# Kernel tuning notes

Hardware: AMD Instinct MI355X
Metric: run time of the kernel (lower is better)

The kernel has to match this reference:

```python
import jax, jax.numpy as jnp
import numpy as np

D_MODEL = 64
D_K = 64
D_V = 64
N_HEADS = 4
D_FF = 64
D_HALF = 32  # d_model / 2 in the sca_* MLPs


def _layer_norm(x, eps=1e-5):
    m = jnp.mean(x, axis=-1, keepdims=True)
    v = jnp.var(x, axis=-1, keepdims=True)
    return (x - m) / jnp.sqrt(v + eps)


def _sca(u, w1, w2):
    # nn.Sequential(Linear(64,32), ReLU, Linear(32,1)), no bias
    return jax.nn.relu(u @ w1) @ w2  # [B,1,1]


def setup_inputs() -> dict:
    key = jax.random.key(0)
    ks = jax.random.split(key, 20)
    B, L = 128, 512

    def lin(k, fan_in, fan_out):
        bound = 1.0 / np.sqrt(fan_in)
        return jax.random.uniform(k, (fan_in, fan_out), jnp.float32, -bound, bound)

    inp = {
        "input": jax.random.normal(ks[0], (B, L, D_MODEL), jnp.float32),
        "attn_mask": jax.random.bernoulli(ks[1], 0.1, (B, L, L)),
        "input_u": jax.random.normal(ks[2], (B, 1, D_MODEL), jnp.float32),
        "W_Q": lin(ks[3], D_MODEL, N_HEADS * D_K),
        "W_K": lin(ks[4], D_MODEL, N_HEADS * D_K),
        "W_V": lin(ks[5], D_MODEL, N_HEADS * D_V),
        "U_Q": lin(ks[6], D_MODEL, D_K),
        "U_K": lin(ks[7], D_MODEL, D_K),
        "U_V": lin(ks[8], D_MODEL, D_V),
        "sq1": lin(ks[9], D_MODEL, D_HALF),
        "sq2": lin(ks[10], D_HALF, 1),
        "sk1": lin(ks[11], D_MODEL, D_HALF),
        "sk2": lin(ks[12], D_HALF, 1),
        "sv1": lin(ks[13], D_MODEL, D_HALF),
        "sv2": lin(ks[14], D_HALF, 1),
        "fc": lin(ks[15], N_HEADS * D_V, D_MODEL),
        "ff1": lin(ks[16], D_MODEL, D_FF),
        "ff2": lin(ks[17], D_FF, D_MODEL),
    }
    return inp


def reference(input, attn_mask, input_u, W_Q, W_K, W_V, U_Q, U_K, U_V,
              sq1, sq2, sk1, sk2, sv1, sv2, fc, ff1, ff2):
    B, L, _ = input.shape
    scale = 1.0 / np.sqrt(D_K).astype(np.float32)

    # multi-head projections: [B, H, L, d]
    Q = (input @ W_Q).reshape(B, L, N_HEADS, D_K).transpose(0, 2, 1, 3)
    K = (input @ W_K).reshape(B, L, N_HEADS, D_K).transpose(0, 2, 1, 3)
    V = (input @ W_V).reshape(B, L, N_HEADS, D_V).transpose(0, 2, 1, 3)

    # per-batch scalar gates from input_u: [B,1,1]
    s_q = _sca(input_u, sq1, sq2)
    s_k = _sca(input_u, sk1, sk2)
    s_v = _sca(input_u, sv1, sv2)

    # single-head u projections, gated; broadcast over heads later
    u_Q = (input @ U_Q) * s_q  # [B, L, d_k]
    u_K = (input @ U_K) * s_k  # [B, L, d_k]
    u_V = (input @ U_V) * s_v  # [B, L, d_v]

    scores = jnp.einsum('bhqd,bhkd->bhqk', Q, K) * scale
    scores = scores + (jnp.einsum('bqd,bkd->bqk', u_Q, u_K) * scale)[:, None]
    scores = jnp.where(attn_mask[:, None], jnp.float32(-1e9), scores)
    attn = jax.nn.softmax(scores, axis=-1)  # [B, H, L, L]

    context = jnp.einsum('bhqk,bhkd->bhqd', attn, V + u_V[:, None])
    context = context.transpose(0, 2, 1, 3).reshape(B, L, N_HEADS * D_V)

    out = context @ fc  # dropout is identity in eval
    enc = _layer_norm(out + input)

    # position-wise FFN with residual + layernorm
    ffn = jax.nn.relu(enc @ ff1) @ ff2
    enc_outputs = _layer_norm(ffn + enc)
    return (enc_outputs, attn)
```

## Files before the change

kernel.cpp:

```cpp
#include <hip/hip_runtime.h>

typedef unsigned char  u8;
typedef unsigned short u16;
typedef unsigned int   u32;

typedef __attribute__((ext_vector_type(8))) short bf16x8;
typedef __attribute__((ext_vector_type(4))) float f32x4;

__device__ __forceinline__ u16 f2bf(float f) {
  union { float f; u32 u; } v; v.f = f;
  u32 u = v.u;
  u32 r = u + 0x7fffu + ((u >> 16) & 1u);
  return (u16)(r >> 16);
}
__device__ __forceinline__ bf16x8 pack8(float4 a, float4 b) {
  bf16x8 r;
  r[0] = (short)f2bf(a.x); r[1] = (short)f2bf(a.y);
  r[2] = (short)f2bf(a.z); r[3] = (short)f2bf(a.w);
  r[4] = (short)f2bf(b.x); r[5] = (short)f2bf(b.y);
  r[6] = (short)f2bf(b.z); r[7] = (short)f2bf(b.w);
  return r;
}
__device__ __forceinline__ f32x4 mfma16(bf16x8 a, bf16x8 b, f32x4 c) {
  return __builtin_amdgcn_mfma_f32_16x16x32_bf16(a, b, c, 0, 0, 0);
}

__global__ void kflaginit(u32* flags) { flags[0] = 0; flags[1] = 0; }

__global__ void kscan(const u32* __restrict__ m, u32* __restrict__ flags) {
  int gid = blockIdx.x * 256 + threadIdx.x;
  const uint4* p = (const uint4*)m;
  u32 gt = 0, fp = 0;
#pragma unroll
  for (int i = 0; i < 4; ++i) {
    uint4 v = p[gid * 4 + i];
    gt |= (u32)((v.x > 1u) | (v.y > 1u) | (v.z > 1u) | (v.w > 1u));
    fp |= (u32)((v.x == 0x3F800000u) | (v.y == 0x3F800000u) |
                (v.z == 0x3F800000u) | (v.w == 0x3F800000u));
  }
  if (gt) flags[0] = 1;
  if (fp) flags[1] = 1;
}

__global__ void kconv(const void* __restrict__ m, const u32* __restrict__ flags,
                      u8* __restrict__ out) {
  int gid = blockIdx.x * 256 + threadIdx.x;
  u32 isf = flags[1], isb = flags[0];
  uchar4 o;
  if (isf) {
    float4 v = ((const float4*)m)[gid];
    o.x = v.x != 0.f; o.y = v.y != 0.f; o.z = v.z != 0.f; o.w = v.w != 0.f;
  } else if (isb) {
    uchar4 v = ((const uchar4*)m)[gid];
    o.x = v.x != 0; o.y = v.y != 0; o.z = v.z != 0; o.w = v.w != 0;
  } else {
    uint4 v = ((const uint4*)m)[gid];
    o.x = v.x != 0; o.y = v.y != 0; o.z = v.z != 0; o.w = v.w != 0;
  }
  ((uchar4*)out)[gid] = o;
}

__global__ void kprep(const float* __restrict__ wq, const float* __restrict__ wk,
                      const float* __restrict__ wv, const float* __restrict__ uq,
                      const float* __restrict__ uk, const float* __restrict__ uv,
                      const float* __restrict__ fc, const float* __restrict__ f1,
                      const float* __restrict__ f2, const float* __restrict__ iu,
                      const float* __restrict__ q1, const float* __restrict__ q2,
                      const float* __restrict__ k1, const float* __restrict__ k2,
                      const float* __restrict__ v1, const float* __restrict__ v2,
                      u16* __restrict__ wqT, u16* __restrict__ wkT, u16* __restrict__ wvT,
                      u16* __restrict__ uqT, u16* __restrict__ ukT, u16* __restrict__ uvT,
                      u16* __restrict__ fcT, u16* __restrict__ f1T, u16* __restrict__ f2T,
                      float* __restrict__ gates) {
  int bid = blockIdx.x, t = threadIdx.x;
  if (bid < 3) {
    const float* src = bid == 0 ? wq : bid == 1 ? wk : wv;
    u16* dst = bid == 0 ? wqT : bid == 1 ? wkT : wvT;
    for (int i = 0; i < 64; ++i) {
      int e = t + i * 256; int n = e & 255, k = e >> 8;
      dst[n * 64 + k] = f2bf(src[k * 256 + n]);
    }
  } else if (bid < 6) {
    const float* src = bid == 3 ? uq : bid == 4 ? uk : uv;
    u16* dst = bid == 3 ? uqT : bid == 4 ? ukT : uvT;
    for (int i = 0; i < 16; ++i) {
      int e = t + i * 256; int n = e & 63, k = e >> 6;
      dst[n * 64 + k] = f2bf(src[k * 64 + n]);
    }
  } else if (bid == 6) {
    for (int i = 0; i < 64; ++i) {
      int e = t + i * 256; int n = e & 63, k = e >> 6;
      fcT[n * 256 + k] = f2bf(fc[k * 64 + n]);
    }
  } else if (bid == 7) {
    for (int i = 0; i < 16; ++i) {
      int e = t + i * 256; int n = e & 63, k = e >> 6;
      f1T[n * 64 + k] = f2bf(f1[k * 64 + n]);
    }
  } else if (bid == 8) {
    for (int i = 0; i < 16; ++i) {
      int e = t + i * 256; int n = e & 63, k = e >> 6;
      f2T[n * 64 + k] = f2bf(f2[k * 64 + n]);
    }
  } else {
    int b = bid - 9;
    __shared__ float u[64];
    if (t < 64) u[t] = iu[b * 64 + t];
    __syncthreads();
    if (t < 64) {
      const float* w1[3] = {q1, k1, v1};
      const float* w2[3] = {q2, k2, v2};
#pragma unroll
      for (int m = 0; m < 3; ++m) {
        float p = 0.f;
        if (t < 32) {
          float h = 0.f;
          for (int i = 0; i < 64; ++i) h += u[i] * w1[m][i * 32 + t];
          p = fmaxf(h, 0.f) * w2[m][t];
        }
        for (int off = 32; off >= 1; off >>= 1) p += __shfl_xor(p, off);
        if (t == 0) gates[m * 128 + b] = p;
      }
    }
  }
}

__launch_bounds__(256, 2)
__global__ void kproj_qk(const float* __restrict__ x,
                         const u16* __restrict__ wqT, const u16* __restrict__ uqT,
                         const u16* __restrict__ wkT, const u16* __restrict__ ukT,
                         const float* __restrict__ gates,
                         u16* __restrict__ qc, u16* __restrict__ qu,
                         u16* __restrict__ kc, u16* __restrict__ ku) {
  __shared__ u16 XT[64 * 136];
  int b = blockIdx.x >> 3, l0 = (blockIdx.x & 7) * 64, t = threadIdx.x;
  {
    int tok = t >> 2, i0 = (t & 3) * 16;
    const float4* s = (const float4*)(x + ((size_t)(b * 512 + l0 + tok)) * 64 + i0);
    *(bf16x8*)&XT[tok * 136 + i0]     = pack8(s[0], s[1]);
    *(bf16x8*)&XT[tok * 136 + i0 + 8] = pack8(s[2], s[3]);
  }
  __syncthreads();

  int w = t >> 6, lane = t & 63, lrow = lane & 15, lgrp = lane >> 4;
  bf16x8 af[4][2];
#pragma unroll
  for (int m = 0; m < 4; ++m)
#pragma unroll
    for (int fs = 0; fs < 2; ++fs)
      af[m][fs] = *(const bf16x8*)&XT[(m * 16 + lrow) * 136 + fs * 32 + lgrp * 8];

  float sq = gates[b], sk = gates[128 + b];
  const f32x4 fz = {0.f, 0.f, 0.f, 0.f};
#pragma unroll
  for (int part = 0; part < 2; ++part) {
    const u16* WT = part ? wkT : wqT;
    const u16* UT = part ? ukT : uqT;
    f32x4 acc[4][5];
#pragma unroll
    for (int m = 0; m < 4; ++m)
#pragma unroll
      for (int nt = 0; nt < 5; ++nt) acc[m][nt] = fz;
#pragma unroll
    for (int fs = 0; fs < 2; ++fs)
#pragma unroll
      for (int nt = 0; nt < 5; ++nt) {
        const u16* src = (nt < 4) ? WT + (w * 64 + nt * 16 + lrow) * 64
                                  : UT + (w * 16 + lrow) * 64;
        bf16x8 bf = *(const bf16x8*)(src + fs * 32 + lgrp * 8);
#pragma unroll
        for (int m = 0; m < 4; ++m)
          acc[m][nt] = mfma16(af[m][fs], bf, acc[m][nt]);
      }
    u16* dstC = part ? kc : qc;
    u16* dstU = part ? ku : qu;
    float presc = part ? 1.0f : 0.125f;
    float gg = (part ? sk : sq) * presc;
#pragma unroll
    for (int nt = 0; nt < 5; ++nt) {
#pragma unroll
      for (int m = 0; m < 4; ++m)
#pragma unroll
        for (int j = 0; j < 4; ++j) {
          int l = l0 + m * 16 + lgrp * 4 + j;
          float v = acc[m][nt][j];
          if (nt < 4) {
            int ncol = w * 64 + nt * 16 + lrow;
            dstC[(((size_t)(b * 4 + (ncol >> 6)) * 512) + l) * 64 + (ncol & 63)] = (short)f2bf(v * presc);
          } else {
            int uc = w * 16 + lrow;
            dstU[((size_t)b * 512 + l) * 64 + uc] = (short)f2bf(v * gg);
          }
        }
    }
  }
}

__launch_bounds__(256, 2)
__global__ void kproj_v(const float* __restrict__ x,
                        const u16* __restrict__ wvT, const u16* __restrict__ uvT,
                        const float* __restrict__ gates, u16* __restrict__ vpt) {
  __shared__ u16 XT[64 * 136];
  __shared__ float Vs[64 * 329];
  int b = blockIdx.x >> 3, l0 = (blockIdx.x & 7) * 64, t = threadIdx.x;
  {
    int tok = t >> 2, i0 = (t & 3) * 16;
    const float4* s = (const float4*)(x + ((size_t)(b * 512 + l0 + tok)) * 64 + i0);
    *(bf16x8*)&XT[tok * 136 + i0]     = pack8(s[0], s[1]);
    *(bf16x8*)&XT[tok * 136 + i0 + 8] = pack8(s[2], s[3]);
  }
  __syncthreads();

  int w = t >> 6, lane = t & 63, lrow = lane & 15, lgrp = lane >> 4;
  bf16x8 af[4][2];
#pragma unroll
  for (int m = 0; m < 4; ++m)
#pragma unroll
    for (int fs = 0; fs < 2; ++fs)
      af[m][fs] = *(const bf16x8*)&XT[(m * 16 + lrow) * 136 + fs * 32 + lgrp * 8];

  const f32x4 fz = {0.f, 0.f, 0.f, 0.f};
  f32x4 acc[4][5];
#pragma unroll
  for (int m = 0; m < 4; ++m)
#pragma unroll
    for (int nt = 0; nt < 5; ++nt) acc[m][nt] = fz;
#pragma unroll
  for (int fs = 0; fs < 2; ++fs)
#pragma unroll
    for (int nt = 0; nt < 5; ++nt) {
      const u16* src = (nt < 4) ? wvT + (w * 64 + nt * 16 + lrow) * 64
                                : uvT + (w * 16 + lrow) * 64;
      bf16x8 bf = *(const bf16x8*)(src + fs * 32 + lgrp * 8);
#pragma unroll
      for (int m = 0; m < 4; ++m)
        acc[m][nt] = mfma16(af[m][fs], bf, acc[m][nt]);
    }
#pragma unroll
  for (int nt = 0; nt < 5; ++nt)
#pragma unroll
    for (int m = 0; m < 4; ++m)
#pragma unroll
      for (int j = 0; j < 4; ++j) {
        int tok = m * 16 + lgrp * 4 + j;
        int col = (nt < 4) ? (w * 64 + nt * 16 + lrow) : (256 + w * 16 + lrow);
        Vs[tok * 329 + col] = acc[m][nt][j];
      }
  __syncthreads();

  float sv = gates[256 + b];
#pragma unroll
  for (int p = 0; p < 4; ++p) {
    int hd = p * 64 + (t >> 2);
    int d = hd & 63;
    int tok0 = (t & 3) * 16;
    bf16x8 v0, v1;
#pragma unroll
    for (int i = 0; i < 8; ++i) {
      int tok = tok0 + i;
      v0[i] = (short)f2bf(Vs[tok * 329 + hd] + Vs[tok * 329 + 256 + d] * sv);
    }
#pragma unroll
    for (int i = 0; i < 8; ++i) {
      int tok = tok0 + 8 + i;
      v1[i] = (short)f2bf(Vs[tok * 329 + hd] + Vs[tok * 329 + 256 + d] * sv);
    }
    size_t base = (((size_t)(b * 4 + (hd >> 6)) * 64) + d) * 512 + l0 + tok0;
    *(bf16x8*)&vpt[base] = v0;
    *(bf16x8*)&vpt[base + 8] = v1;
  }
}

__launch_bounds__(512)
__global__ void __attribute__((amdgpu_waves_per_eu(2, 4)))
kattn(const u16* __restrict__ qc, const u16* __restrict__ qu,
      const u16* __restrict__ kc, const u16* __restrict__ ku,
      const u16* __restrict__ vpt, const u8* __restrict__ maskb,
      float* __restrict__ aout, u16* __restrict__ ctx) {
  __shared__ char smem[35840];
  u16* KT  = (u16*)smem;
  u16* Pl0 = (u16*)smem;
  u16* Pl1 = (u16*)(smem + 17408);
  float* SMm = (float*)(smem + 34816);
  float* SMl = (float*)(smem + 35328);

  int bid = blockIdx.x;
  int logical = (bid & 7) * 512 + (bid >> 3);
  int b = logical >> 5;
  int r5 = logical & 31;
  int qt = r5 >> 2, hh = r5 & 3;
  int bh = b * 4 + hh;
  int q0 = qt * 64;

  int t = threadIdx.x, w = t >> 6, lane = t & 63, lrow = lane & 15, lgrp = lane >> 4;
  int qsub = w & 3, g = w >> 2, g64 = g * 64;
  int qloc0 = qsub * 16 + lgrp * 4;

  bf16x8 qf[4];
  {
    const u16* qrow = qc + ((size_t)bh * 512 + q0 + qsub * 16 + lrow) * 64;
    const u16* urow = qu + ((size_t)b  * 512 + q0 + qsub * 16 + lrow) * 64;
    qf[0] = *(const bf16x8*)(qrow + lgrp * 8);
    qf[1] = *(const bf16x8*)(qrow + 32 + lgrp * 8);
    qf[2] = *(const bf16x8*)(urow + lgrp * 8);
    qf[3] = *(const bf16x8*)(urow + 32 + lgrp * 8);
  }

  int r = t >> 2;
  uint4 kreg[4];
#define LDK(kt)                                                                   \
  {                                                                               \
    _Pragma("unroll")                                                             \
    for (int i = 0; i < 4; ++i) {                                                 \
      int c = (t & 3) * 4 + i;                                                    \
      const u16* src = (c < 8)                                                    \
        ? kc + ((size_t)bh * 512 + (kt) * 128 + r) * 64 + c * 8                   \
        : ku + ((size_t)b  * 512 + (kt) * 128 + r) * 64 + (c - 8) * 8;            \
      kreg[i] = *(const uint4*)src;                                               \
    }                                                                             \
  }

  LDK(0);
  const f32x4 fz = {0.f, 0.f, 0.f, 0.f};
  f32x4 acc[16];
#pragma unroll
  for (int i = 0; i < 16; ++i) acc[i] = fz;

#pragma unroll
  for (int kt = 0; kt < 4; ++kt) {
    __syncthreads();
#pragma unroll
    for (int i = 0; i < 4; ++i)
      *(uint4*)&KT[r * 136 + ((t & 3) * 4 + i) * 8] = kreg[i];
    if (kt < 3) LDK(kt + 1);
    __syncthreads();
#pragma unroll
    for (int fs = 0; fs < 4; ++fs)
#pragma unroll
      for (int nt = 0; nt < 4; ++nt) {
        bf16x8 bf = *(const bf16x8*)&KT[(g64 + nt * 16 + lrow) * 136 + fs * 32 + lgrp * 8];
        acc[kt * 4 + nt] = mfma16(qf[fs], bf, acc[kt * 4 + nt]);
      }
  }

  const u8* mrow = maskb + ((size_t)b * 512 + q0 + qloc0) * 512;
  float mj[4] = {-3.0e38f, -3.0e38f, -3.0e38f, -3.0e38f};
#pragma unroll
  for (int i = 0; i < 16; ++i) {
    int kpos = (i >> 2) * 128 + g64 + (i & 3) * 16 + lrow;
#pragma unroll
    for (int j = 0; j < 4; ++j) {
      float s = acc[i][j];
      if (mrow[(size_t)j * 512 + kpos]) s = -1.0e9f;
      acc[i][j] = s;
      mj[j] = fmaxf(mj[j], s);
    }
  }
#pragma unroll
  for (int j = 0; j < 4; ++j) {
    mj[j] = fmaxf(mj[j], __shfl_xor(mj[j], 1));
    mj[j] = fmaxf(mj[j], __shfl_xor(mj[j], 2));
    mj[j] = fmaxf(mj[j], __shfl_xor(mj[j], 4));
    mj[j] = fmaxf(mj[j], __shfl_xor(mj[j], 8));
  }
  if (lrow == 0) {
#pragma unroll
    for (int j = 0; j < 4; ++j) SMm[g64 + qloc0 + j] = mj[j];
  }
  __syncthreads();
  float gm[4];
#pragma unroll
  for (int j = 0; j < 4; ++j) gm[j] = fmaxf(SMm[qloc0 + j], SMm[64 + qloc0 + j]);
  float lj[4] = {0.f, 0.f, 0.f, 0.f};
#pragma unroll
  for (int i = 0; i < 16; ++i)
#pragma unroll
    for (int j = 0; j < 4; ++j) {
      float p = __expf(acc[i][j] - gm[j]);
      acc[i][j] = p;
      lj[j] += p;
    }
#pragma unroll
  for (int j = 0; j < 4; ++j) {
    lj[j] += __shfl_xor(lj[j], 1);
    lj[j] += __shfl_xor(lj[j], 2);
    lj[j] += __shfl_xor(lj[j], 4);
    lj[j] += __shfl_xor(lj[j], 8);
  }
  if (lrow == 0) {
#pragma unroll
    for (int j = 0; j < 4; ++j) SMl[g64 + qloc0 + j] = lj[j];
  }
  __syncthreads();
  float inv[4];
#pragma unroll
  for (int j = 0; j < 4; ++j) inv[j] = 1.0f / (SMl[qloc0 + j] + SMl[64 + qloc0 + j]);

  size_t ab = ((size_t)bh * 512 + q0 + qloc0) * 512;
  f32x4 cacc[2] = {fz, fz};
#pragma unroll
  for (int c = 0; c < 4; ++c) {
    u16* Pl = (c & 1) ? Pl1 : Pl0;
    bf16x8 vf[4][2];
#pragma unroll
    for (int ks = 0; ks < 4; ++ks)
#pragma unroll
      for (int nt2 = 0; nt2 < 2; ++nt2)
        vf[ks][nt2] = *(const bf16x8*)(vpt + ((size_t)bh * 64 + g * 32 + nt2 * 16 + lrow) * 512
                                       + c * 128 + ks * 32 + lgrp * 8);
#pragma unroll
    for (int nt = 0; nt < 4; ++nt)
#pragma unroll
      for (int j = 0; j < 4; ++j)
        Pl[(qloc0 + j) * 136 + g64 + nt * 16 + lrow] = (short)f2bf(acc[c * 4 + nt][j] * inv[j]);
    __syncthreads();
#pragma unroll
    for (int nt = 0; nt < 4; ++nt)
#pragma unroll
      for (int j = 0; j < 4; ++j)
        aout[ab + (size_t)j * 512 + c * 128 + g64 + nt * 16 + lrow] = acc[c * 4 + nt][j] * inv[j];
#pragma unroll
    for (int ks = 0; ks < 4; ++ks) {
      bf16x8 a = *(const bf16x8*)&Pl[(qsub * 16 + lrow) * 136 + ks * 32 + lgrp * 8];
      cacc[0] = mfma16(a, vf[ks][0], cacc[0]);
      cacc[1] = mfma16(a, vf[ks][1], cacc[1]);
    }
  }
#pragma unroll
  for (int nt2 = 0; nt2 < 2; ++nt2)
#pragma unroll
    for (int j = 0; j < 4; ++j)
      ctx[((size_t)b * 512 + q0 + qloc0 + j) * 256 + hh * 64 + g * 32 + nt2 * 16 + lrow] =
          (short)f2bf(cacc[nt2][j]);
}

__launch_bounds__(256, 2)
__global__ void kffn(const u16* __restrict__ ctx, const float* __restrict__ x,
                     const u16* __restrict__ fcT, const u16* __restrict__ f1T,
                     const u16* __restrict__ f2T, float* __restrict__ out) {
  __shared__ float ENC[64 * 68];
  __shared__ u16 EBF[64 * 72];
  __shared__ u16 HBF[64 * 72];
  int b = blockIdx.x >> 3, l0 = (blockIdx.x & 7) * 64, t = threadIdx.x;
  int w = t >> 6, lane = t & 63, lrow = lane & 15, lgrp = lane >> 4;
  int row = w * 16 + lgrp * 4;
  const f32x4 fz = {0.f, 0.f, 0.f, 0.f};

  f32x4 acc[4];
#pragma unroll
  for (int nt = 0; nt < 4; ++nt) acc[nt] = fz;
#pragma unroll
  for (int ks = 0; ks < 8; ++ks) {
    bf16x8 a = *(const bf16x8*)(ctx + ((size_t)(b * 512 + l0 + w * 16 + lrow)) * 256 + ks * 32 + lgrp * 8);
#pragma unroll
    for (int nt = 0; nt < 4; ++nt) {
      bf16x8 bf = *(const bf16x8*)(fcT + (nt * 16 + lrow) * 256 + ks * 32 + lgrp * 8);
      acc[nt] = mfma16(a, bf, acc[nt]);
    }
  }
  const float* xb = x + ((size_t)(b * 512 + l0)) * 64;
#pragma unroll
  for (int nt = 0; nt < 4; ++nt)
#pragma unroll
    for (int j = 0; j < 4; ++j)
      acc[nt][j] += xb[(row + j) * 64 + nt * 16 + lrow];

  float mean[4], rstd[4];
#pragma unroll
  for (int j = 0; j < 4; ++j) {
    float s = acc[0][j] + acc[1][j] + acc[2][j] + acc[3][j];
    s += __shfl_xor(s, 1); s += __shfl_xor(s, 2); s += __shfl_xor(s, 4); s += __shfl_xor(s, 8);
    mean[j] = s * 0.015625f;
  }
#pragma unroll
  for (int j = 0; j < 4; ++j) {
    float d0 = acc[0][j] - mean[j], d1 = acc[1][j] - mean[j];
    float d2 = acc[2][j] - mean[j], d3 = acc[3][j] - mean[j];
    float s = d0 * d0 + d1 * d1 + d2 * d2 + d3 * d3;
    s += __shfl_xor(s, 1); s += __shfl_xor(s, 2); s += __shfl_xor(s, 4); s += __shfl_xor(s, 8);
    rstd[j] = 1.0f / sqrtf(s * 0.015625f + 1e-5f);
  }
#pragma unroll
  for (int nt = 0; nt < 4; ++nt)
#pragma unroll
    for (int j = 0; j < 4; ++j) {
      float v = (acc[nt][j] - mean[j]) * rstd[j];
      ENC[(row + j) * 68 + nt * 16 + lrow] = v;
      EBF[(row + j) * 72 + nt * 16 + lrow] = (short)f2bf(v);
    }

  f32x4 h4[4];
#pragma unroll
  for (int nt = 0; nt < 4; ++nt) h4[nt] = fz;
#pragma unroll
  for (int ks = 0; ks < 2; ++ks) {
    bf16x8 a = *(const bf16x8*)&EBF[(w * 16 + lrow) * 72 + ks * 32 + lgrp * 8];
#pragma unroll
    for (int nt = 0; nt < 4; ++nt) {
      bf16x8 bf = *(const bf16x8*)(f1T + (nt * 16 + lrow) * 64 + ks * 32 + lgrp * 8);
      h4[nt] = mfma16(a, bf, h4[nt]);
    }
  }
#pragma unroll
  for (int nt = 0; nt < 4; ++nt)
#pragma unroll
    for (int j = 0; j < 4; ++j)
      HBF[(row + j) * 72 + nt * 16 + lrow] = (short)f2bf(fmaxf(h4[nt][j], 0.f));

  f32x4 o4[4];
#pragma unroll
  for (int nt = 0; nt < 4; ++nt) o4[nt] = fz;
#pragma unroll
  for (int ks = 0; ks < 2; ++ks) {
    bf16x8 a = *(const bf16x8*)&HBF[(w * 16 + lrow) * 72 + ks * 32 + lgrp * 8];
#pragma unroll
    for (int nt = 0; nt < 4; ++nt) {
      bf16x8 bf = *(const bf16x8*)(f2T + (nt * 16 + lrow) * 64 + ks * 32 + lgrp * 8);
      o4[nt] = mfma16(a, bf, o4[nt]);
    }
  }
#pragma unroll
  for (int nt = 0; nt < 4; ++nt)
#pragma unroll
    for (int j = 0; j < 4; ++j)
      o4[nt][j] += ENC[(row + j) * 68 + nt * 16 + lrow];

  float mean2[4], rstd2[4];
#pragma unroll
  for (int j = 0; j < 4; ++j) {
    float s = o4[0][j] + o4[1][j] + o4[2][j] + o4[3][j];
    s += __shfl_xor(s, 1); s += __shfl_xor(s, 2); s += __shfl_xor(s, 4); s += __shfl_xor(s, 8);
    mean2[j] = s * 0.015625f;
  }
#pragma unroll
  for (int j = 0; j < 4; ++j) {
    float d0 = o4[0][j] - mean2[j], d1 = o4[1][j] - mean2[j];
    float d2 = o4[2][j] - mean2[j], d3 = o4[3][j] - mean2[j];
    float s = d0 * d0 + d1 * d1 + d2 * d2 + d3 * d3;
    s += __shfl_xor(s, 1); s += __shfl_xor(s, 2); s += __shfl_xor(s, 4); s += __shfl_xor(s, 8);
    rstd2[j] = 1.0f / sqrtf(s * 0.015625f + 1e-5f);
  }
#pragma unroll
  for (int nt = 0; nt < 4; ++nt)
#pragma unroll
    for (int j = 0; j < 4; ++j)
      out[((size_t)(b * 512 + l0) + row + j) * 64 + nt * 16 + lrow] =
          (o4[nt][j] - mean2[j]) * rstd2[j];
}

extern "C" void kernel_launch(void* const* d_in, const int* in_sizes, int n_in,
                              void* d_out, int out_size, void* d_ws, size_t ws_size,
                              hipStream_t stream) {
  const float* x   = (const float*)d_in[0];
  const void*  msk = d_in[1];
  const float* iu  = (const float*)d_in[2];
  const float* wq  = (const float*)d_in[3];
  const float* wk  = (const float*)d_in[4];
  const float* wv  = (const float*)d_in[5];
  const float* uq  = (const float*)d_in[6];
  const float* uk  = (const float*)d_in[7];
  const float* uv  = (const float*)d_in[8];
  const float* q1  = (const float*)d_in[9];
  const float* q2  = (const float*)d_in[10];
  const float* k1  = (const float*)d_in[11];
  const float* k2  = (const float*)d_in[12];
  const float* v1  = (const float*)d_in[13];
  const float* v2  = (const float*)d_in[14];
  const float* fcw = (const float*)d_in[15];
  const float* f1w = (const float*)d_in[16];
  const float* f2w = (const float*)d_in[17];
  float* out = (float*)d_out;

  char* ws = (char*)d_ws;
  u32*   flags = (u32*)ws;
  float* gates = (float*)(ws + 64);
  u16* wqT = (u16*)(ws + 4096);
  u16* wkT = (u16*)(ws + 36864);
  u16* wvT = (u16*)(ws + 69632);
  u16* uqT = (u16*)(ws + 102400);
  u16* ukT = (u16*)(ws + 110592);
  u16* uvT = (u16*)(ws + 118784);
  u16* fcT = (u16*)(ws + 126976);
  u16* f1T = (u16*)(ws + 159744);
  u16* f2T = (u16*)(ws + 167936);
  u16* qc  = (u16*)(ws + 180224);
  u16* qu  = (u16*)(ws + 33734656);
  u16* kc  = (u16*)(ws + 42123264);
  u16* ku  = (u16*)(ws + 75677696);
  u16* vpt = (u16*)(ws + 84066304);
  u8*  mb  = (u8*) (ws + 117620736);
  u16* ctx = (u16*)(ws + 151175168);

  kflaginit<<<dim3(1), dim3(1), 0, stream>>>(flags);
  kscan<<<dim3(1024), dim3(256), 0, stream>>>((const u32*)msk, flags);
  kconv<<<dim3(32768), dim3(256), 0, stream>>>(msk, flags, mb);
  kprep<<<dim3(137), dim3(256), 0, stream>>>(wq, wk, wv, uq, uk, uv, fcw, f1w, f2w,
                                             iu, q1, q2, k1, k2, v1, v2,
                                             wqT, wkT, wvT, uqT, ukT, uvT, fcT, f1T, f2T, gates);
  kproj_qk<<<dim3(1024), dim3(256), 0, stream>>>(x, wqT, uqT, wkT, ukT, gates, qc, qu, kc, ku);
  kproj_v<<<dim3(1024), dim3(256), 0, stream>>>(x, wvT, uvT, gates, vpt);
  kattn<<<dim3(4096), dim3(512), 0, stream>>>(qc, qu, kc, ku, vpt, mb, out + 4194304, ctx);
  kffn<<<dim3(1024), dim3(256), 0, stream>>>(ctx, x, fcT, f1T, f2T, out);
}
```

Before: 477.8 us.

## Keep full K head resident in LDS and loop all query tiles per block

```diff
diff --git a/kernel.cpp b/kernel.cpp
--- a/kernel.cpp
+++ b/kernel.cpp
@@ -272,166 +272,175 @@
 }
 
 __launch_bounds__(512)
-__global__ void __attribute__((amdgpu_waves_per_eu(2, 4)))
+__global__ void __attribute__((amdgpu_waves_per_eu(2, 2)))
 kattn(const u16* __restrict__ qc, const u16* __restrict__ qu,
       const u16* __restrict__ kc, const u16* __restrict__ ku,
       const u16* __restrict__ vpt, const u8* __restrict__ maskb,
       float* __restrict__ aout, u16* __restrict__ ctx) {
-  __shared__ char smem[35840];
-  u16* KT  = (u16*)smem;
-  u16* Pl0 = (u16*)smem;
-  u16* Pl1 = (u16*)(smem + 17408);
-  float* SMm = (float*)(smem + 34816);
-  float* SMl = (float*)(smem + 35328);
+  __shared__ char smem[163840];
+  char* Kl  = smem;
+  char* Pl0 = smem + 131072;
+  char* Pl1 = smem + 147456;
+  float* SMm = (float*)(smem + 147456);
+  float* SMl = (float*)(smem + 147968);
 
   int bid = blockIdx.x;
-  int logical = (bid & 7) * 512 + (bid >> 3);
-  int b = logical >> 5;
-  int r5 = logical & 31;
-  int qt = r5 >> 2, hh = r5 & 3;
+  int logical = (bid & 7) * 64 + (bid >> 3);
+  int b = logical >> 2, hh = logical & 3;
   int bh = b * 4 + hh;
-  int q0 = qt * 64;
 
   int t = threadIdx.x, w = t >> 6, lane = t & 63, lrow = lane & 15, lgrp = lane >> 4;
-  int qsub = w & 3, g = w >> 2, g64 = g * 64;
+  int qsub = w & 3, g = w >> 2;
   int qloc0 = qsub * 16 + lgrp * 4;
-
-  bf16x8 qf[4];
+  int lswz = (lrow & 7) << 4;
+
   {
-    const u16* qrow = qc + ((size_t)bh * 512 + q0 + qsub * 16 + lrow) * 64;
-    const u16* urow = qu + ((size_t)b  * 512 + q0 + qsub * 16 + lrow) * 64;
-    qf[0] = *(const bf16x8*)(qrow + lgrp * 8);
-    qf[1] = *(const bf16x8*)(qrow + 32 + lgrp * 8);
-    qf[2] = *(const bf16x8*)(urow + lgrp * 8);
-    qf[3] = *(const bf16x8*)(urow + 32 + lgrp * 8);
-  }
-
-  int r = t >> 2;
-  uint4 kreg[4];
-#define LDK(kt)                                                                   \
-  {                                                                               \
-    _Pragma("unroll")                                                             \
-    for (int i = 0; i < 4; ++i) {                                                 \
-      int c = (t & 3) * 4 + i;                                                    \
-      const u16* src = (c < 8)                                                    \
-        ? kc + ((size_t)bh * 512 + (kt) * 128 + r) * 64 + c * 8                   \
-        : ku + ((size_t)b  * 512 + (kt) * 128 + r) * 64 + (c - 8) * 8;            \
-      kreg[i] = *(const uint4*)src;                                               \
-    }                                                                             \
-  }
-
-  LDK(0);
+    int r = t;
+    const u16* kr = kc + ((size_t)bh * 512 + r) * 64;
+    const u16* ur = ku + ((size_t)b  * 512 + r) * 64;
+    int rbase = r * 256, rswz = (r & 7) << 4;
+#pragma unroll
+    for (int q = 0; q < 8; ++q)
+      *(uint4*)&Kl[rbase + ((q * 16) ^ rswz)] = *(const uint4*)(kr + q * 8);
+#pragma unroll
+    for (int q = 8; q < 16; ++q)
+      *(uint4*)&Kl[rbase + ((q * 16) ^ rswz)] = *(const uint4*)(ur + (q - 8) * 8);
+  }
+  __syncthreads();
+
   const f32x4 fz = {0.f, 0.f, 0.f, 0.f};
-  f32x4 acc[16];
-#pragma unroll
-  for (int i = 0; i < 16; ++i) acc[i] = fz;
-
-#pragma unroll
-  for (int kt = 0; kt < 4; ++kt) {
+
+  for (int qi = 0; qi < 8; ++qi) {
+    int q0 = qi * 64;
+
+    bf16x8 qf[4];
+    {
+      const u16* qrow = qc + ((size_t)bh * 512 + q0 + qsub * 16 + lrow) * 64;
+      const u16* urow = qu + ((size_t)b  * 512 + q0 + qsub * 16 + lrow) * 64;
+      qf[0] = *(const bf16x8*)(qrow + lgrp * 8);
+      qf[1] = *(const bf16x8*)(qrow + 32 + lgrp * 8);
+      qf[2] = *(const bf16x8*)(urow + lgrp * 8);
+      qf[3] = *(const bf16x8*)(urow + 32 + lgrp * 8);
+    }
+
+    f32x4 acc[16];
+#pragma unroll
+    for (int i = 0; i < 16; ++i) acc[i] = fz;
+#pragma unroll
+    for (int fs = 0; fs < 4; ++fs) {
+      int cb = (fs * 64 + lgrp * 16) ^ lswz;
+#pragma unroll
+      for (int nt = 0; nt < 16; ++nt) {
+        int kpos = g * 256 + nt * 16 + lrow;
+        bf16x8 bf = *(const bf16x8*)&Kl[kpos * 256 + cb];
+        acc[nt] = mfma16(qf[fs], bf, acc[nt]);
+      }
+    }
+
+    const u8* mrow = maskb + ((size_t)b * 512 + q0 + qloc0) * 512;
+    float mj[4] = {-3.0e38f, -3.0e38f, -3.0e38f, -3.0e38f};
+#pragma unroll
+    for (int i = 0; i < 16; ++i) {
+      int kpos = g * 256 + i * 16 + lrow;
+#pragma unroll
+      for (int j = 0; j < 4; ++j) {
+        float s = acc[i][j];
+        if (mrow[(size_t)j * 512 + kpos]) s = -1.0e9f;
+        acc[i][j] = s;
+        mj[j] = fmaxf(mj[j], s);
+      }
+    }
+#pragma unroll
+    for (int j = 0; j < 4; ++j) {
+      mj[j] = fmaxf(mj[j], __shfl_xor(mj[j], 1));
+      mj[j] = fmaxf(mj[j], __shfl_xor(mj[j], 2));
+      mj[j] = fmaxf(mj[j], __shfl_xor(mj[j], 4));
+      mj[j] = fmaxf(mj[j], __shfl_xor(mj[j], 8));
+    }
     __syncthreads();
-#pragma unroll
-    for (int i = 0; i < 4; ++i)
-      *(uint4*)&KT[r * 136 + ((t & 3) * 4 + i) * 8] = kreg[i];
-    if (kt < 3) LDK(kt + 1);
+    if (lrow == 0) {
+#pragma unroll
+      for (int j = 0; j < 4; ++j) SMm[g * 64 + qloc0 + j] = mj[j];
+    }
     __syncthreads();
-#pragma unroll
-    for (int fs = 0; fs < 4; ++fs)
-#pragma unroll
-      for (int nt = 0; nt < 4; ++nt) {
-        bf16x8 bf = *(const bf16x8*)&KT[(g64 + nt * 16 + lrow) * 136 + fs * 32 + lgrp * 8];
-        acc[kt * 4 + nt] = mfma16(qf[fs], bf, acc[kt * 4 + nt]);
-      }
-  }
-
-  const u8* mrow = maskb + ((size_t)b * 512 + q0 + qloc0) * 512;
-  float mj[4] = {-3.0e38f, -3.0e38f, -3.0e38f, -3.0e38f};
-#pragma unroll
-  for (int i = 0; i < 16; ++i) {
-    int kpos = (i >> 2) * 128 + g64 + (i & 3) * 16 + lrow;
+    float gm[4];
+#pragma unroll
+    for (int j = 0; j < 4; ++j) gm[j] = fmaxf(SMm[qloc0 + j], SMm[64 + qloc0 + j]);
+    float lj[4] = {0.f, 0.f, 0.f, 0.f};
+#pragma unroll
+    for (int i = 0; i < 16; ++i)
+#pragma unroll
+      for (int j = 0; j < 4; ++j) {
+        float p = __expf(acc[i][j] - gm[j]);
+        acc[i][j] = p;
+        lj[j] += p;
+      }
 #pragma unroll
     for (int j = 0; j < 4; ++j) {
-      float s = acc[i][j];
-      if (mrow[(size_t)j * 512 + kpos]) s = -1.0e9f;
-      acc[i][j] = s;
-      mj[j] = fmaxf(mj[j], s);
-    }
-  }
-#pragma unroll
-  for (int j = 0; j < 4; ++j) {
-    mj[j] = fmaxf(mj[j], __shfl_xor(mj[j], 1));
-    mj[j] = fmaxf(mj[j], __shfl_xor(mj[j], 2));
-    mj[j] = fmaxf(mj[j], __shfl_xor(mj[j], 4));
-    mj[j] = fmaxf(mj[j], __shfl_xor(mj[j], 8));
-  }
-  if (lrow == 0) {
-#pragma unroll
-    for (int j = 0; j < 4; ++j) SMm[g64 + qloc0 + j] = mj[j];
-  }
-  __syncthreads();
-  float gm[4];
-#pragma unroll
-  for (int j = 0; j < 4; ++j) gm[j] = fmaxf(SMm[qloc0 + j], SMm[64 + qloc0 + j]);
-  float lj[4] = {0.f, 0.f, 0.f, 0.f};
-#pragma unroll
-  for (int i = 0; i < 16; ++i)
-#pragma unroll
-    for (int j = 0; j < 4; ++j) {
-      float p = __expf(acc[i][j] - gm[j]);
-      acc[i][j] = p;
-      lj[j] += p;
-    }
-#pragma unroll
-  for (int j = 0; j < 4; ++j) {
-    lj[j] += __shfl_xor(lj[j], 1);
-    lj[j] += __shfl_xor(lj[j], 2);
-    lj[j] += __shfl_xor(lj[j], 4);
-    lj[j] += __shfl_xor(lj[j], 8);
-  }
-  if (lrow == 0) {
-#pragma unroll
-    for (int j = 0; j < 4; ++j) SMl[g64 + qloc0 + j] = lj[j];
-  }
-  __syncthreads();
-  float inv[4];
-#pragma unroll
-  for (int j = 0; j < 4; ++j) inv[j] = 1.0f / (SMl[qloc0 + j] + SMl[64 + qloc0 + j]);
-
-  size_t ab = ((size_t)bh * 512 + q0 + qloc0) * 512;
-  f32x4 cacc[2] = {fz, fz};
-#pragma unroll
-  for (int c = 0; c < 4; ++c) {
-    u16* Pl = (c & 1) ? Pl1 : Pl0;
-    bf16x8 vf[4][2];
-#pragma unroll
-    for (int ks = 0; ks < 4; ++ks)
-#pragma unroll
-      for (int nt2 = 0; nt2 < 2; ++nt2)
-        vf[ks][nt2] = *(const bf16x8*)(vpt + ((size_t)bh * 64 + g * 32 + nt2 * 16 + lrow) * 512
-                                       + c * 128 + ks * 32 + lgrp * 8);
-#pragma unroll
-    for (int nt = 0; nt < 4; ++nt)
+      lj[j] += __shfl_xor(lj[j], 1);
+      lj[j] += __shfl_xor(lj[j], 2);
+      lj[j] += __shfl_xor(lj[j], 4);
+      lj[j] += __shfl_xor(lj[j], 8);
+    }
+    if (lrow == 0) {
+#pragma unroll
+      for (int j = 0; j < 4; ++j) SMl[g * 64 + qloc0 + j] = lj[j];
+    }
+    __syncthreads();
+    float inv[4];
+#pragma unroll
+    for (int j = 0; j < 4; ++j) inv[j] = 1.0f / (SMl[qloc0 + j] + SMl[64 + qloc0 + j]);
+
+    size_t ab = ((size_t)bh * 512 + q0 + qloc0) * 512;
+    f32x4 cacc[2] = {fz, fz};
+#pragma unroll
+    for (int c = 0; c < 4; ++c) {
+      char* Pl = (c & 1) ? Pl1 : Pl0;
+      bf16x8 vf[4][2];
+#pragma unroll
+      for (int ks = 0; ks < 4; ++ks)
+#pragma unroll
+        for (int nt2 = 0; nt2 < 2; ++nt2)
+          vf[ks][nt2] = *(const bf16x8*)(vpt + ((size_t)bh * 64 + g * 32 + nt2 * 16 + lrow) * 512
+                                         + c * 128 + ks * 32 + lgrp * 8);
+      int iw = (c >> 1);
+      int ibase = (c & 1) * 8;
+      if (g == iw) {
+#pragma unroll
+        for (int i2 = 0; i2 < 8; ++i2)
+#pragma unroll
+          for (int j = 0; j < 4; ++j) {
+            int row = qloc0 + j;
+            int kk = i2 * 16 + lrow;
+            *(u16*)&Pl[row * 256 + ((kk * 2) ^ ((row & 7) << 4))] =
+                f2bf(acc[ibase + i2][j] * inv[j]);
+          }
+      }
+      __syncthreads();
+      if (g == iw) {
+#pragma unroll
+        for (int i2 = 0; i2 < 8; ++i2)
+#pragma unroll
+          for (int j = 0; j < 4; ++j)
+            aout[ab + (size_t)j * 512 + c * 128 + i2 * 16 + lrow] =
+                acc[ibase + i2][j] * inv[j];
+      }
+      int arow = qsub * 16 + lrow;
+      int acb = arow * 256;
+#pragma unroll
+      for (int ks = 0; ks < 4; ++ks) {
+        bf16x8 a = *(const bf16x8*)&Pl[acb + ((ks * 64 + lgrp * 16) ^ lswz)];
+        cacc[0] = mfma16(a, vf[ks][0], cacc[0]);
+        cacc[1] = mfma16(a, vf[ks][1], cacc[1]);
+      }
+    }
+#pragma unroll
+    for (int nt2 = 0; nt2 < 2; ++nt2)
 #pragma unroll
       for (int j = 0; j < 4; ++j)
-        Pl[(qloc0 + j) * 136 + g64 + nt * 16 + lrow] = (short)f2bf(acc[c * 4 + nt][j] * inv[j]);
-    __syncthreads();
-#pragma unroll
-    for (int nt = 0; nt < 4; ++nt)
-#pragma unroll
-      for (int j = 0; j < 4; ++j)
-        aout[ab + (size_t)j * 512 + c * 128 + g64 + nt * 16 + lrow] = acc[c * 4 + nt][j] * inv[j];
-#pragma unroll
-    for (int ks = 0; ks < 4; ++ks) {
-      bf16x8 a = *(const bf16x8*)&Pl[(qsub * 16 + lrow) * 136 + ks * 32 + lgrp * 8];
-      cacc[0] = mfma16(a, vf[ks][0], cacc[0]);
-      cacc[1] = mfma16(a, vf[ks][1], cacc[1]);
-    }
-  }
-#pragma unroll
-  for (int nt2 = 0; nt2 < 2; ++nt2)
-#pragma unroll
-    for (int j = 0; j < 4; ++j)
-      ctx[((size_t)b * 512 + q0 + qloc0 + j) * 256 + hh * 64 + g * 32 + nt2 * 16 + lrow] =
-          (short)f2bf(cacc[nt2][j]);
+        ctx[((size_t)b * 512 + q0 + qloc0 + j) * 256 + hh * 64 + g * 32 + nt2 * 16 + lrow] =
+            (short)f2bf(cacc[nt2][j]);
+  }
 }
 
 __launch_bounds__(256, 2)
@@ -599,6 +608,6 @@
                                              wqT, wkT, wvT, uqT, ukT, uvT, fcT, f1T, f2T, gates);
   kproj_qk<<<dim3(1024), dim3(256), 0, stream>>>(x, wqT, uqT, wkT, ukT, gates, qc, qu, kc, ku);
   kproj_v<<<dim3(1024), dim3(256), 0, stream>>>(x, wvT, uvT, gates, vpt);
-  kattn<<<dim3(4096), dim3(512), 0, stream>>>(qc, qu, kc, ku, vpt, mb, out + 4194304, ctx);
+  kattn<<<dim3(512), dim3(512), 0, stream>>>(qc, qu, kc, ku, vpt, mb, out + 4194304, ctx);
   kffn<<<dim3(1024), dim3(256), 0, stream>>>(ctx, x, fcT, f1T, f2T, out);
 }
```

New measurement: 858.6 us. 1.8x slower.

## Load K fragments directly from global and defer attention-probability stores to the end

Applied to the files above, without the earlier changes.

```diff
diff --git a/kernel.cpp b/kernel.cpp
--- a/kernel.cpp
+++ b/kernel.cpp
@@ -278,7 +278,6 @@
       const u16* __restrict__ vpt, const u8* __restrict__ maskb,
       float* __restrict__ aout, u16* __restrict__ ctx) {
   __shared__ char smem[35840];
-  u16* KT  = (u16*)smem;
   u16* Pl0 = (u16*)smem;
   u16* Pl1 = (u16*)(smem + 17408);
   float* SMm = (float*)(smem + 34816);
@@ -293,7 +292,7 @@
   int q0 = qt * 64;
 
   int t = threadIdx.x, w = t >> 6, lane = t & 63, lrow = lane & 15, lgrp = lane >> 4;
-  int qsub = w & 3, g = w >> 2, g64 = g * 64;
+  int qsub = w & 3, g = w >> 2;
   int qloc0 = qsub * 16 + lgrp * 4;
 
   bf16x8 qf[4];
@@ -306,48 +305,35 @@
     qf[3] = *(const bf16x8*)(urow + 32 + lgrp * 8);
   }
 
-  int r = t >> 2;
-  uint4 kreg[4];
-#define LDK(kt)                                                                   \
-  {                                                                               \
-    _Pragma("unroll")                                                             \
-    for (int i = 0; i < 4; ++i) {                                                 \
-      int c = (t & 3) * 4 + i;                                                    \
-      const u16* src = (c < 8)                                                    \
-        ? kc + ((size_t)bh * 512 + (kt) * 128 + r) * 64 + c * 8                   \
-        : ku + ((size_t)b  * 512 + (kt) * 128 + r) * 64 + (c - 8) * 8;            \
-      kreg[i] = *(const uint4*)src;                                               \
-    }                                                                             \
-  }
-
-  LDK(0);
   const f32x4 fz = {0.f, 0.f, 0.f, 0.f};
   f32x4 acc[16];
 #pragma unroll
   for (int i = 0; i < 16; ++i) acc[i] = fz;
 
-#pragma unroll
-  for (int kt = 0; kt < 4; ++kt) {
-    __syncthreads();
-#pragma unroll
-    for (int i = 0; i < 4; ++i)
-      *(uint4*)&KT[r * 136 + ((t & 3) * 4 + i) * 8] = kreg[i];
-    if (kt < 3) LDK(kt + 1);
-    __syncthreads();
-#pragma unroll
-    for (int fs = 0; fs < 4; ++fs)
-#pragma unroll
-      for (int nt = 0; nt < 4; ++nt) {
-        bf16x8 bf = *(const bf16x8*)&KT[(g64 + nt * 16 + lrow) * 136 + fs * 32 + lgrp * 8];
-        acc[kt * 4 + nt] = mfma16(qf[fs], bf, acc[kt * 4 + nt]);
-      }
+  {
+    const u16* kbase = kc + (size_t)bh * 512 * 64;
+    const u16* ubase = ku + (size_t)b  * 512 * 64;
+#pragma unroll
+    for (int nt = 0; nt < 16; ++nt) {
+      int kpos = g * 256 + nt * 16 + lrow;
+      const u16* krow_ = kbase + (size_t)kpos * 64;
+      const u16* urow_ = ubase + (size_t)kpos * 64;
+      bf16x8 b0 = *(const bf16x8*)(krow_ + lgrp * 8);
+      bf16x8 b1 = *(const bf16x8*)(krow_ + 32 + lgrp * 8);
+      bf16x8 b2 = *(const bf16x8*)(urow_ + lgrp * 8);
+      bf16x8 b3 = *(const bf16x8*)(urow_ + 32 + lgrp * 8);
+      acc[nt] = mfma16(qf[0], b0, acc[nt]);
+      acc[nt] = mfma16(qf[1], b1, acc[nt]);
+      acc[nt] = mfma16(qf[2], b2, acc[nt]);
+      acc[nt] = mfma16(qf[3], b3, acc[nt]);
+    }
   }
 
   const u8* mrow = maskb + ((size_t)b * 512 + q0 + qloc0) * 512;
   float mj[4] = {-3.0e38f, -3.0e38f, -3.0e38f, -3.0e38f};
 #pragma unroll
   for (int i = 0; i < 16; ++i) {
-    int kpos = (i >> 2) * 128 + g64 + (i & 3) * 16 + lrow;
+    int kpos = g * 256 + i * 16 + lrow;
 #pragma unroll
     for (int j = 0; j < 4; ++j) {
       float s = acc[i][j];
@@ -365,7 +351,7 @@
   }
   if (lrow == 0) {
 #pragma unroll
-    for (int j = 0; j < 4; ++j) SMm[g64 + qloc0 + j] = mj[j];
+    for (int j = 0; j < 4; ++j) SMm[g * 64 + qloc0 + j] = mj[j];
   }
   __syncthreads();
   float gm[4];
@@ -389,14 +375,13 @@
   }
   if (lrow == 0) {
 #pragma unroll
-    for (int j = 0; j < 4; ++j) SMl[g64 + qloc0 + j] = lj[j];
+    for (int j = 0; j < 4; ++j) SMl[g * 64 + qloc0 + j] = lj[j];
   }
   __syncthreads();
   float inv[4];
 #pragma unroll
   for (int j = 0; j < 4; ++j) inv[j] = 1.0f / (SMl[qloc0 + j] + SMl[64 + qloc0 + j]);
 
-  size_t ab = ((size_t)bh * 512 + q0 + qloc0) * 512;
   f32x4 cacc[2] = {fz, fz};
 #pragma unroll
   for (int c = 0; c < 4; ++c) {
@@ -408,17 +393,15 @@
       for (int nt2 = 0; nt2 < 2; ++nt2)
         vf[ks][nt2] = *(const bf16x8*)(vpt + ((size_t)bh * 64 + g * 32 + nt2 * 16 + lrow) * 512
                                        + c * 128 + ks * 32 + lgrp * 8);
-#pragma unroll
-    for (int nt = 0; nt < 4; ++nt)
-#pragma unroll
-      for (int j = 0; j < 4; ++j)
-        Pl[(qloc0 + j) * 136 + g64 + nt * 16 + lrow] = (short)f2bf(acc[c * 4 + nt][j] * inv[j]);
+    int iw = c >> 1, ibase = (c & 1) * 8;
+    if (g == iw) {
+#pragma unroll
+      for (int i2 = 0; i2 < 8; ++i2)
+#pragma unroll
+        for (int j = 0; j < 4; ++j)
+          Pl[(qloc0 + j) * 136 + i2 * 16 + lrow] = (short)f2bf(acc[ibase + i2][j] * inv[j]);
+    }
     __syncthreads();
-#pragma unroll
-    for (int nt = 0; nt < 4; ++nt)
-#pragma unroll
-      for (int j = 0; j < 4; ++j)
-        aout[ab + (size_t)j * 512 + c * 128 + g64 + nt * 16 + lrow] = acc[c * 4 + nt][j] * inv[j];
 #pragma unroll
     for (int ks = 0; ks < 4; ++ks) {
       bf16x8 a = *(const bf16x8*)&Pl[(qsub * 16 + lrow) * 136 + ks * 32 + lgrp * 8];
@@ -426,12 +409,22 @@
       cacc[1] = mfma16(a, vf[ks][1], cacc[1]);
     }
   }
+
 #pragma unroll
   for (int nt2 = 0; nt2 < 2; ++nt2)
 #pragma unroll
     for (int j = 0; j < 4; ++j)
       ctx[((size_t)b * 512 + q0 + qloc0 + j) * 256 + hh * 64 + g * 32 + nt2 * 16 + lrow] =
           (short)f2bf(cacc[nt2][j]);
+
+  size_t ab = ((size_t)bh * 512 + q0 + qloc0) * 512;
+#pragma unroll
+  for (int i = 0; i < 16; ++i) {
+    int kpos = g * 256 + i * 16 + lrow;
+#pragma unroll
+    for (int j = 0; j < 4; ++j)
+      aout[ab + (size_t)j * 512 + kpos] = acc[i][j] * inv[j];
+  }
 }
 
 __launch_bounds__(256, 2)
```

After: 632.3 us. +32.4%, slower.

## Pack attention mask into bitmask and read bit words in attention kernel

Applied to the files above, without the earlier changes.

```diff
diff --git a/kernel.cpp b/kernel.cpp
--- a/kernel.cpp
+++ b/kernel.cpp
@@ -42,22 +42,47 @@
   if (fp) flags[1] = 1;
 }
 
-__global__ void kconv(const void* __restrict__ m, const u32* __restrict__ flags,
-                      u8* __restrict__ out) {
+__global__ void kpack(const void* __restrict__ m, const u32* __restrict__ flags,
+                      u32* __restrict__ bits) {
   int gid = blockIdx.x * 256 + threadIdx.x;
   u32 isf = flags[1], isb = flags[0];
-  uchar4 o;
-  if (isf) {
-    float4 v = ((const float4*)m)[gid];
-    o.x = v.x != 0.f; o.y = v.y != 0.f; o.z = v.z != 0.f; o.w = v.w != 0.f;
-  } else if (isb) {
-    uchar4 v = ((const uchar4*)m)[gid];
-    o.x = v.x != 0; o.y = v.y != 0; o.z = v.z != 0; o.w = v.w != 0;
+  u32 w = 0;
+  if (isb) {
+    const uint4* p = (const uint4*)m + (size_t)gid * 2;
+#pragma unroll
+    for (int q = 0; q < 2; ++q) {
+      uint4 v = p[q];
+      u32 x0 = v.x, x1 = v.y, x2 = v.z, x3 = v.w;
+#pragma unroll
+      for (int k2 = 0; k2 < 4; ++k2) {
+        w |= (u32)(((x0 >> (k2 * 8)) & 255u) != 0u) << (q * 16 + 0 * 4 + k2);
+        w |= (u32)(((x1 >> (k2 * 8)) & 255u) != 0u) << (q * 16 + 1 * 4 + k2);
+        w |= (u32)(((x2 >> (k2 * 8)) & 255u) != 0u) << (q * 16 + 2 * 4 + k2);
+        w |= (u32)(((x3 >> (k2 * 8)) & 255u) != 0u) << (q * 16 + 3 * 4 + k2);
+      }
+    }
+  } else if (isf) {
+    const float4* p = (const float4*)m + (size_t)gid * 8;
+#pragma unroll
+    for (int q = 0; q < 8; ++q) {
+      float4 v = p[q];
+      w |= (u32)(v.x != 0.f) << (q * 4 + 0);
+      w |= (u32)(v.y != 0.f) << (q * 4 + 1);
+      w |= (u32)(v.z != 0.f) << (q * 4 + 2);
+      w |= (u32)(v.w != 0.f) << (q * 4 + 3);
+    }
   } else {
-    uint4 v = ((const uint4*)m)[gid];
-    o.x = v.x != 0; o.y = v.y != 0; o.z = v.z != 0; o.w = v.w != 0;
-  }
-  ((uchar4*)out)[gid] = o;
+    const uint4* p = (const uint4*)m + (size_t)gid * 8;
+#pragma unroll
+    for (int q = 0; q < 8; ++q) {
+      uint4 v = p[q];
+      w |= (u32)(v.x != 0u) << (q * 4 + 0);
+      w |= (u32)(v.y != 0u) << (q * 4 + 1);
+      w |= (u32)(v.z != 0u) << (q * 4 + 2);
+      w |= (u32)(v.w != 0u) << (q * 4 + 3);
+    }
+  }
+  bits[gid] = w;
 }
 
 __global__ void kprep(const float* __restrict__ wq, const float* __restrict__ wk,
@@ -272,10 +297,10 @@
 }
 
 __launch_bounds__(512)
-__global__ void __attribute__((amdgpu_waves_per_eu(2, 4)))
+__global__ void __attribute__((amdgpu_waves_per_eu(2, 6)))
 kattn(const u16* __restrict__ qc, const u16* __restrict__ qu,
       const u16* __restrict__ kc, const u16* __restrict__ ku,
-      const u16* __restrict__ vpt, const u8* __restrict__ maskb,
+      const u16* __restrict__ vpt, const u32* __restrict__ mbits,
       float* __restrict__ aout, u16* __restrict__ ctx) {
   __shared__ char smem[35840];
   u16* KT  = (u16*)smem;
@@ -343,17 +368,25 @@
       }
   }
 
-  const u8* mrow = maskb + ((size_t)b * 512 + q0 + qloc0) * 512;
+  const u32* brow = mbits + ((size_t)(b * 512 + q0 + qloc0)) * 16;
   float mj[4] = {-3.0e38f, -3.0e38f, -3.0e38f, -3.0e38f};
 #pragma unroll
-  for (int i = 0; i < 16; ++i) {
-    int kpos = (i >> 2) * 128 + g64 + (i & 3) * 16 + lrow;
-#pragma unroll
-    for (int j = 0; j < 4; ++j) {
-      float s = acc[i][j];
-      if (mrow[(size_t)j * 512 + kpos]) s = -1.0e9f;
-      acc[i][j] = s;
-      mj[j] = fmaxf(mj[j], s);
+  for (int c = 0; c < 4; ++c) {
+    uint2 mw[4];
+#pragma unroll
+    for (int j = 0; j < 4; ++j)
+      mw[j] = *(const uint2*)(brow + j * 16 + c * 4 + g * 2);
+#pragma unroll
+    for (int s = 0; s < 4; ++s) {
+      int i = c * 4 + s;
+#pragma unroll
+      for (int j = 0; j < 4; ++j) {
+        u32 word = (s < 2) ? mw[j].x : mw[j].y;
+        float v = acc[i][j];
+        if ((word >> ((s & 1) * 16 + lrow)) & 1u) v = -1.0e9f;
+        acc[i][j] = v;
+        mj[j] = fmaxf(mj[j], v);
+      }
     }
   }
 #pragma unroll
@@ -588,17 +621,17 @@
   u16* kc  = (u16*)(ws + 42123264);
   u16* ku  = (u16*)(ws + 75677696);
   u16* vpt = (u16*)(ws + 84066304);
-  u8*  mb  = (u8*) (ws + 117620736);
+  u32* mbits = (u32*)(ws + 117620736);
   u16* ctx = (u16*)(ws + 151175168);
 
   kflaginit<<<dim3(1), dim3(1), 0, stream>>>(flags);
   kscan<<<dim3(1024), dim3(256), 0, stream>>>((const u32*)msk, flags);
-  kconv<<<dim3(32768), dim3(256), 0, stream>>>(msk, flags, mb);
+  kpack<<<dim3(4096), dim3(256), 0, stream>>>(msk, flags, mbits);
   kprep<<<dim3(137), dim3(256), 0, stream>>>(wq, wk, wv, uq, uk, uv, fcw, f1w, f2w,
                                              iu, q1, q2, k1, k2, v1, v2,
                                              wqT, wkT, wvT, uqT, ukT, uvT, fcT, f1T, f2T, gates);
   kproj_qk<<<dim3(1024), dim3(256), 0, stream>>>(x, wqT, uqT, wkT, ukT, gates, qc, qu, kc, ku);
   kproj_v<<<dim3(1024), dim3(256), 0, stream>>>(x, wvT, uvT, gates, vpt);
-  kattn<<<dim3(4096), dim3(512), 0, stream>>>(qc, qu, kc, ku, vpt, mb, out + 4194304, ctx);
+  kattn<<<dim3(4096), dim3(512), 0, stream>>>(qc, qu, kc, ku, vpt, mbits, out + 4194304, ctx);
   kffn<<<dim3(1024), dim3(256), 0, stream>>>(ctx, x, fcT, f1T, f2T, out);
 }
```

After: 564.7 us. 1.18x slower.
